# Optimization experiments

Hardware: AMD Instinct MI355X
Metric: run time of the kernel (lower is better)

## Reference

```python
import jax, jax.numpy as jnp
import numpy as np

T, B, D_IN, NHID = 4096, 8, 512, 512

def setup_inputs() -> dict:
    key = jax.random.key(0)
    k1, k2, k3 = jax.random.split(key, 3)
    scale_i = 1.0 / np.sqrt(D_IN)
    scale_h = 1.0 / np.sqrt(NHID)
    x = jax.random.normal(k1, (T, B, D_IN), dtype=jnp.float32)
    hidden0 = jnp.zeros((2, B, NHID), dtype=jnp.float32)  # [h; cell]
    Wi = jax.random.normal(k2, (D_IN, 4 * NHID), dtype=jnp.float32) * scale_i
    bi = jnp.zeros((4 * NHID,), dtype=jnp.float32)
    Wh = jax.random.normal(k3, (NHID, 4 * NHID), dtype=jnp.float32) * scale_h
    bh = jnp.zeros((4 * NHID,), dtype=jnp.float32)
    return {"x": x, "hidden0": hidden0, "Wi": Wi, "bi": bi, "Wh": Wh, "bh": bh}

def reference(x, hidden0, Wi, bi, Wh, bh):
    n = Wh.shape[0]

    def update(state, xt):
        h, cell = state[0], state[1]               # [B, n] each
        pre = xt @ Wi + bi + h @ Wh + bh           # [B, 4n]
        gates = jax.nn.sigmoid(pre[:, : 3 * n])
        forget_gate = gates[:, :n]
        input_gate = gates[:, n : 2 * n]
        output_gate = gates[:, 2 * n : 3 * n]
        new_cell = jnp.tanh(pre[:, 3 * n :])
        cell = forget_gate * cell + input_gate * new_cell
        h = output_gate * jnp.tanh(cell)
        return jnp.stack([h, cell]), h

    new_state, hidden_stacked = jax.lax.scan(update, hidden0, x)
    return hidden_stacked, new_state
```

## Files before the change

kernel.cpp:

```cpp
#include <hip/hip_runtime.h>
#include <hip/hip_bf16.h>

#define T_STEPS 4096
#define BATCH 8
#define DIN 512
#define NH 512
#define G4 2048
#define NWV 32
#define JPW 16

typedef __attribute__((ext_vector_type(8))) short bf16x8;
typedef __attribute__((ext_vector_type(4))) float f32x4;
typedef __attribute__((ext_vector_type(4))) int i32x4;

__device__ __forceinline__ unsigned short f2b(float f) {
  __hip_bfloat16 h = __float2bfloat16(f);
  return __builtin_bit_cast(unsigned short, h);
}
__device__ __forceinline__ float b2f(unsigned short u) {
  unsigned int x = ((unsigned int)u) << 16;
  return __builtin_bit_cast(float, x);
}
__device__ __forceinline__ float sigf(float x) { return 1.f / (1.f + __expf(-x)); }
__device__ __forceinline__ float tanh_fast(float x) { return 1.f - 2.f / (1.f + __expf(2.f * x)); }

__global__ __launch_bounds__(512) void init_ws(const float* __restrict__ h0,
                                               unsigned int* __restrict__ tags,
                                               unsigned short* __restrict__ hbuf) {
  int tid = threadIdx.x;
  if (tid < NWV) tags[tid] = 0u;
  for (int i = tid; i < 4096; i += 512) {
    int b = i >> 9, j = i & 511;
    hbuf[i] = f2b(h0[b * NH + j]);
    hbuf[4096 + i] = 0;
  }
}

#define BM 64
#define BN 64
#define BK 16
__global__ __launch_bounds__(256) void xi_gemm(const float* __restrict__ x,
                                               const float* __restrict__ Wi,
                                               const float* __restrict__ bi,
                                               const float* __restrict__ bh,
                                               unsigned short* __restrict__ xi) {
  __shared__ float As[BK][BM + 4];
  __shared__ float Bs[BK][BN + 4];
  const int tid = threadIdx.x;
  const int m0 = blockIdx.x * BM;
  const int n0 = blockIdx.y * BN;
  const int tx = tid & 15, ty = tid >> 4;
  const int arow = tid & 63, ak = (tid >> 6) << 2;
  const int bk = tid >> 4, bn = (tid & 15) << 2;
  float acc[4][4] = {};
  for (int k0 = 0; k0 < DIN; k0 += BK) {
    float4 av = *(const float4*)(x + (size_t)(m0 + arow) * DIN + k0 + ak);
    float4 bv = *(const float4*)(Wi + (size_t)(k0 + bk) * G4 + n0 + bn);
    __syncthreads();
    As[ak + 0][arow] = av.x;
    As[ak + 1][arow] = av.y;
    As[ak + 2][arow] = av.z;
    As[ak + 3][arow] = av.w;
    *(float4*)&Bs[bk][bn] = bv;
    __syncthreads();
#pragma unroll
    for (int kk = 0; kk < BK; ++kk) {
      float am[4], bw[4];
      *(float4*)am = *(const float4*)&As[kk][ty << 2];
      *(float4*)bw = *(const float4*)&Bs[kk][tx << 2];
#pragma unroll
      for (int i = 0; i < 4; ++i)
#pragma unroll
        for (int j = 0; j < 4; ++j) acc[i][j] = fmaf(am[i], bw[j], acc[i][j]);
    }
  }
  const int m_base = m0 + (ty << 2);
  const int n_base = n0 + (tx << 2);
  const int tt = m_base >> 3;
  const int rg = (m_base & 7) >> 2;
  const int gate = n_base >> 9;
  const int wv = (n_base & 511) >> 4;
  const int col0 = n_base & 15;
#pragma unroll
  for (int j = 0; j < 4; ++j) {
    int n = n_base + j;
    float bs = bi[n] + bh[n];
    unsigned long long pk = 0;
#pragma unroll
    for (int i = 0; i < 4; ++i)
      pk |= (unsigned long long)f2b(acc[i][j] + bs) << (16 * i);
    int lane = rg * 16 + col0 + j;
    size_t u16idx = (((size_t)tt * NWV + wv) * 32 + lane) * 16 + gate * 4;
    *(unsigned long long*)(xi + u16idx) = pk;
  }
}

__global__ __launch_bounds__(64, 1) void lstm_rec(const float* __restrict__ Wh,
                                                  const float* __restrict__ h0c0,
                                                  const unsigned short* __restrict__ xi,
                                                  float* __restrict__ out,
                                                  unsigned int* tags,
                                                  unsigned short* hbuf) {
  const int wv = blockIdx.x;
  const int j0 = wv * JPW;
  const int lane = threadIdx.x;
  const int col = lane & 15;
  const int rg = lane >> 4;

  __shared__ bf16x8 bwS[4][16][64];

  {
    const int gp = lane >> 4, cp = lane & 15;
    const float* wsrc = Wh + (size_t)gp * NH + j0 + cp;
#pragma unroll 4
    for (int k = 0; k < 512; ++k) {
      float wval = wsrc[(size_t)k * G4];
      const int ks = k >> 5, kq = (k >> 3) & 3, e = k & 7;
      ((unsigned short*)&bwS[gp][ks][kq * 16 + cp])[e] = f2b(wval);
    }
  }
  __syncthreads();

  bf16x8 bwR0[16], bwR1[16];
#pragma unroll
  for (int ks = 0; ks < 16; ++ks) {
    bwR0[ks] = bwS[0][ks][lane];
    bwR1[ks] = bwS[1][ks][lane];
  }

  f32x4 cell = {0.f, 0.f, 0.f, 0.f};
  if (lane < 32) {
#pragma unroll
    for (int q = 0; q < 4; ++q)
      cell[q] = h0c0[(size_t)(BATCH + rg * 4 + q) * NH + j0 + col];
  }

  i32x4 xiC0, xiC1, xiN0, xiN1;
  {
    const unsigned short* xp = xi + ((size_t)wv * 32 + (lane & 31)) * 16;
    asm volatile("global_load_dwordx4 %0, %1, off" : "=&v"(xiC0) : "v"(xp));
    asm volatile("global_load_dwordx4 %0, %1, off offset:16" : "=&v"(xiC1) : "v"(xp));
  }
  f32x4 hq = {0.f, 0.f, 0.f, 0.f};

  const unsigned int* tp = tags + (lane & 31);
  unsigned int* myTag = tags + wv;

  for (int t = 0; t < T_STEPS; ++t) {
    {
      unsigned int tv;
      do {
        asm volatile("global_load_dword %0, %1, off sc0 sc1\n\ts_waitcnt vmcnt(0)"
                     : "=v"(tv) : "v"(tp) : "memory");
      } while (__any((int)tv < t));
    }

    const unsigned short* mb = hbuf + ((t & 1) << 12);
    const unsigned short* ap = mb + (col & 7) * 512 + (rg << 3);
    i32x4 afr[16];
    asm volatile("global_load_dwordx4 %0, %1, off sc0 sc1" : "=v"(afr[0]) : "v"(ap));
    asm volatile("global_load_dwordx4 %0, %1, off offset:64 sc0 sc1" : "=v"(afr[1]) : "v"(ap));
    asm volatile("global_load_dwordx4 %0, %1, off offset:128 sc0 sc1" : "=v"(afr[2]) : "v"(ap));
    asm volatile("global_load_dwordx4 %0, %1, off offset:192 sc0 sc1" : "=v"(afr[3]) : "v"(ap));
    asm volatile("global_load_dwordx4 %0, %1, off offset:256 sc0 sc1" : "=v"(afr[4]) : "v"(ap));
    asm volatile("global_load_dwordx4 %0, %1, off offset:320 sc0 sc1" : "=v"(afr[5]) : "v"(ap));
    asm volatile("global_load_dwordx4 %0, %1, off offset:384 sc0 sc1" : "=v"(afr[6]) : "v"(ap));
    asm volatile("global_load_dwordx4 %0, %1, off offset:448 sc0 sc1" : "=v"(afr[7]) : "v"(ap));
    asm volatile("global_load_dwordx4 %0, %1, off offset:512 sc0 sc1" : "=v"(afr[8]) : "v"(ap));
    asm volatile("global_load_dwordx4 %0, %1, off offset:576 sc0 sc1" : "=v"(afr[9]) : "v"(ap));
    asm volatile("global_load_dwordx4 %0, %1, off offset:640 sc0 sc1" : "=v"(afr[10]) : "v"(ap));
    asm volatile("global_load_dwordx4 %0, %1, off offset:704 sc0 sc1" : "=v"(afr[11]) : "v"(ap));
    asm volatile("global_load_dwordx4 %0, %1, off offset:768 sc0 sc1" : "=v"(afr[12]) : "v"(ap));
    asm volatile("global_load_dwordx4 %0, %1, off offset:832 sc0 sc1" : "=v"(afr[13]) : "v"(ap));
    asm volatile("global_load_dwordx4 %0, %1, off offset:896 sc0 sc1" : "=v"(afr[14]) : "v"(ap));
    asm volatile("global_load_dwordx4 %0, %1, off offset:960 sc0 sc1" : "=v"(afr[15]) : "v"(ap));
    asm volatile("s_waitcnt vmcnt(0)" ::: "memory");
    __builtin_amdgcn_sched_barrier(0);

    f32x4 acc[4][2];
    {
      unsigned int wrd[8] = {(unsigned int)xiC0[0], (unsigned int)xiC0[1],
                             (unsigned int)xiC0[2], (unsigned int)xiC0[3],
                             (unsigned int)xiC1[0], (unsigned int)xiC1[1],
                             (unsigned int)xiC1[2], (unsigned int)xiC1[3]};
      f32x4 z = {0.f, 0.f, 0.f, 0.f};
#pragma unroll
      for (int g = 0; g < 4; ++g) {
#pragma unroll
        for (int q = 0; q < 4; ++q) {
          const int idx = g * 4 + q;
          acc[g][0][q] = b2f((unsigned short)(wrd[idx >> 1] >> ((idx & 1) * 16)));
        }
        acc[g][1] = z;
      }
    }
#pragma unroll
    for (int ks = 0; ks < 16; ++ks) {
      bf16x8 a = __builtin_bit_cast(bf16x8, afr[ks]);
      acc[0][ks & 1] = __builtin_amdgcn_mfma_f32_16x16x32_bf16(a, bwR0[ks], acc[0][ks & 1], 0, 0, 0);
      acc[1][ks & 1] = __builtin_amdgcn_mfma_f32_16x16x32_bf16(a, bwR1[ks], acc[1][ks & 1], 0, 0, 0);
      acc[2][ks & 1] = __builtin_amdgcn_mfma_f32_16x16x32_bf16(a, bwS[2][ks][lane], acc[2][ks & 1], 0, 0, 0);
      acc[3][ks & 1] = __builtin_amdgcn_mfma_f32_16x16x32_bf16(a, bwS[3][ks][lane], acc[3][ks & 1], 0, 0, 0);
    }

#pragma unroll
    for (int q = 0; q < 4; ++q) {
      float pf = acc[0][0][q] + acc[0][1][q];
      float pi = acc[1][0][q] + acc[1][1][q];
      float po = acc[2][0][q] + acc[2][1][q];
      float pg = acc[3][0][q] + acc[3][1][q];
      float fg = sigf(pf), ig = sigf(pi), og = sigf(po), gg = tanh_fast(pg);
      float cn = fg * cell[q] + ig * gg;
      cell[q] = cn;
      hq[q] = og * tanh_fast(cn);
    }

    if (lane < 32) {
      unsigned short* pp = hbuf + (((t + 1) & 1) << 12) + (rg * 4) * 512 + j0 + col;
      unsigned int h0u = f2b(hq[0]), h1u = f2b(hq[1]), h2u = f2b(hq[2]), h3u = f2b(hq[3]);
      asm volatile("global_store_short %0, %1, off sc0 sc1" :: "v"(pp), "v"(h0u) : "memory");
      asm volatile("global_store_short %0, %1, off offset:1024 sc0 sc1" :: "v"(pp), "v"(h1u) : "memory");
      asm volatile("global_store_short %0, %1, off offset:2048 sc0 sc1" :: "v"(pp), "v"(h2u) : "memory");
      asm volatile("global_store_short %0, %1, off offset:3072 sc0 sc1" :: "v"(pp), "v"(h3u) : "memory");
    }
    asm volatile("s_waitcnt vmcnt(0)" ::: "memory");
    if (lane == 0) {
      unsigned int tn1 = (unsigned int)(t + 1);
      asm volatile("global_store_dword %0, %1, off sc0 sc1" :: "v"(myTag), "v"(tn1) : "memory");
    }

    if (lane < 32) {
#pragma unroll
      for (int q = 0; q < 4; ++q)
        out[((size_t)t * BATCH + (rg * 4 + q)) * NH + j0 + col] = hq[q];
    }
    {
      const int tn = (t + 1 < T_STEPS) ? (t + 1) : t;
      const unsigned short* xp = xi + (((size_t)tn * NWV + wv) * 32 + (lane & 31)) * 16;
      asm volatile("global_load_dwordx4 %0, %1, off" : "=&v"(xiN0) : "v"(xp));
      asm volatile("global_load_dwordx4 %0, %1, off offset:16" : "=&v"(xiN1) : "v"(xp));
    }
    xiC0 = xiN0;
    xiC1 = xiN1;
  }

  if (lane < 32) {
    const size_t tail = (size_t)T_STEPS * BATCH * NH;
#pragma unroll
    for (int q = 0; q < 4; ++q) {
      out[tail + (size_t)(rg * 4 + q) * NH + j0 + col] = hq[q];
      out[tail + (size_t)BATCH * NH + (size_t)(rg * 4 + q) * NH + j0 + col] = cell[q];
    }
  }
}

extern "C" void kernel_launch(void* const* d_in, const int* in_sizes, int n_in,
                              void* d_out, int out_size, void* d_ws, size_t ws_size,
                              hipStream_t stream) {
  const float* x  = (const float*)d_in[0];
  const float* h0 = (const float*)d_in[1];
  const float* Wi = (const float*)d_in[2];
  const float* bi = (const float*)d_in[3];
  const float* Wh = (const float*)d_in[4];
  const float* bh = (const float*)d_in[5];
  float* out = (float*)d_out;

  unsigned int* tags = (unsigned int*)d_ws;
  unsigned short* hbuf = (unsigned short*)((char*)d_ws + 256);
  unsigned short* xi = (unsigned short*)((char*)d_ws + 65536);

  init_ws<<<1, 512, 0, stream>>>(h0, tags, hbuf);
  dim3 g1((T_STEPS * BATCH) / BM, G4 / BN);
  xi_gemm<<<g1, 256, 0, stream>>>(x, Wi, bi, bh, xi);
  lstm_rec<<<NWV, 64, 0, stream>>>(Wh, h0, xi, out, tags, hbuf);
}
```

Measured before the change: 15.11 ms.

## Replace flag polling with tagged mailbox carrying hidden state and step tag

Removes the separate per-workgroup tag array. Each published bf16 hidden pair is now stored next to its timestep tag in an 8-byte mailbox word, so consumers poll the data loads themselves and retry until every tag matches. This drops one round-trip (flag poll, then data load) per recurrent step. It also batches the output writes through shared memory, flushing 16 timesteps with float4 stores, and issues the next xi prefetch earlier. The costs are double the data loaded per poll and a bounded retry loop that gives up silently after 4096 rounds.

```diff
diff --git a/kernel.cpp b/kernel.cpp
--- a/kernel.cpp
+++ b/kernel.cpp
@@ -25,14 +25,14 @@
 __device__ __forceinline__ float tanh_fast(float x) { return 1.f - 2.f / (1.f + __expf(2.f * x)); }
 
 __global__ __launch_bounds__(512) void init_ws(const float* __restrict__ h0,
-                                               unsigned int* __restrict__ tags,
-                                               unsigned short* __restrict__ hbuf) {
+                                               unsigned long long* __restrict__ mbox) {
   int tid = threadIdx.x;
-  if (tid < NWV) tags[tid] = 0u;
-  for (int i = tid; i < 4096; i += 512) {
-    int b = i >> 9, j = i & 511;
-    hbuf[i] = f2b(h0[b * NH + j]);
-    hbuf[4096 + i] = 0;
+  for (int i = tid; i < 2048; i += 512) {
+    int b = i >> 8, m = i & 255;
+    unsigned int pk = ((unsigned int)f2b(h0[b * NH + 2 * m + 1]) << 16) |
+                      f2b(h0[b * NH + 2 * m]);
+    mbox[i] = (unsigned long long)pk;
+    mbox[2048 + i] = 0xFFFFFFFFull << 32;
   }
 }
 
@@ -99,8 +99,7 @@
                                                   const float* __restrict__ h0c0,
                                                   const unsigned short* __restrict__ xi,
                                                   float* __restrict__ out,
-                                                  unsigned int* tags,
-                                                  unsigned short* hbuf) {
+                                                  unsigned long long* mbox) {
   const int wv = blockIdx.x;
   const int j0 = wv * JPW;
   const int lane = threadIdx.x;
@@ -108,6 +107,7 @@
   const int rg = lane >> 4;
 
   __shared__ bf16x8 bwS[4][16][64];
+  __shared__ float obuf[16][8][16];
 
   {
     const int gp = lane >> 4, cp = lane & 15;
@@ -143,39 +143,55 @@
   }
   f32x4 hq = {0.f, 0.f, 0.f, 0.f};
 
-  const unsigned int* tp = tags + (lane & 31);
-  unsigned int* myTag = tags + wv;
+  const char* mbase = (const char*)mbox + (size_t)(col & 7) * 2048 + (size_t)rg * 32;
+  const int pb = lane >> 2, pu = lane & 3;
+  const int srcbase = ((pb >> 2) << 4) + (pu << 2);
+  const int qs = pb & 3;
+  char* pbase = (char*)mbox + (size_t)pb * 2048 + (size_t)j0 * 4 + (size_t)pu * 16;
+
+  i32x4 aL[16], aH[16];
 
   for (int t = 0; t < T_STEPS; ++t) {
+    const unsigned int tgt = (unsigned int)t;
+    const char* mb = mbase + ((t & 1) << 14);
+
+#define PL(i, o0, o1)                                                              \
+    asm volatile("global_load_dwordx4 %0, %1, off offset:" #o0 " sc0 sc1"          \
+                 : "=&v"(aL[i]) : "v"(mb));                                        \
+    asm volatile("global_load_dwordx4 %0, %1, off offset:" #o1 " sc0 sc1"          \
+                 : "=&v"(aH[i]) : "v"(mb));
+#define ISSUE_ALL                                                                  \
+    PL(0, 0, 16)       PL(1, 128, 144)    PL(2, 256, 272)    PL(3, 384, 400)       \
+    PL(4, 512, 528)    PL(5, 640, 656)    PL(6, 768, 784)    PL(7, 896, 912)       \
+    PL(8, 1024, 1040)  PL(9, 1152, 1168)  PL(10, 1280, 1296) PL(11, 1408, 1424)    \
+    PL(12, 1536, 1552) PL(13, 1664, 1680) PL(14, 1792, 1808) PL(15, 1920, 1936)
     {
-      unsigned int tv;
-      do {
-        asm volatile("global_load_dword %0, %1, off sc0 sc1\n\ts_waitcnt vmcnt(0)"
-                     : "=v"(tv) : "v"(tp) : "memory");
-      } while (__any((int)tv < t));
-    }
-
-    const unsigned short* mb = hbuf + ((t & 1) << 12);
-    const unsigned short* ap = mb + (col & 7) * 512 + (rg << 3);
-    i32x4 afr[16];
-    asm volatile("global_load_dwordx4 %0, %1, off sc0 sc1" : "=v"(afr[0]) : "v"(ap));
-    asm volatile("global_load_dwordx4 %0, %1, off offset:64 sc0 sc1" : "=v"(afr[1]) : "v"(ap));
-    asm volatile("global_load_dwordx4 %0, %1, off offset:128 sc0 sc1" : "=v"(afr[2]) : "v"(ap));
-    asm volatile("global_load_dwordx4 %0, %1, off offset:192 sc0 sc1" : "=v"(afr[3]) : "v"(ap));
-    asm volatile("global_load_dwordx4 %0, %1, off offset:256 sc0 sc1" : "=v"(afr[4]) : "v"(ap));
-    asm volatile("global_load_dwordx4 %0, %1, off offset:320 sc0 sc1" : "=v"(afr[5]) : "v"(ap));
-    asm volatile("global_load_dwordx4 %0, %1, off offset:384 sc0 sc1" : "=v"(afr[6]) : "v"(ap));
-    asm volatile("global_load_dwordx4 %0, %1, off offset:448 sc0 sc1" : "=v"(afr[7]) : "v"(ap));
-    asm volatile("global_load_dwordx4 %0, %1, off offset:512 sc0 sc1" : "=v"(afr[8]) : "v"(ap));
-    asm volatile("global_load_dwordx4 %0, %1, off offset:576 sc0 sc1" : "=v"(afr[9]) : "v"(ap));
-    asm volatile("global_load_dwordx4 %0, %1, off offset:640 sc0 sc1" : "=v"(afr[10]) : "v"(ap));
-    asm volatile("global_load_dwordx4 %0, %1, off offset:704 sc0 sc1" : "=v"(afr[11]) : "v"(ap));
-    asm volatile("global_load_dwordx4 %0, %1, off offset:768 sc0 sc1" : "=v"(afr[12]) : "v"(ap));
-    asm volatile("global_load_dwordx4 %0, %1, off offset:832 sc0 sc1" : "=v"(afr[13]) : "v"(ap));
-    asm volatile("global_load_dwordx4 %0, %1, off offset:896 sc0 sc1" : "=v"(afr[14]) : "v"(ap));
-    asm volatile("global_load_dwordx4 %0, %1, off offset:960 sc0 sc1" : "=v"(afr[15]) : "v"(ap));
-    asm volatile("s_waitcnt vmcnt(0)" ::: "memory");
-    __builtin_amdgcn_sched_barrier(0);
+      unsigned int bad;
+      int rounds = 0;
+      for (;;) {
+        ISSUE_ALL
+        asm volatile("s_waitcnt vmcnt(0)" ::: "memory");
+        __builtin_amdgcn_sched_barrier(0);
+        bad = 0u;
+#pragma unroll
+        for (int ks = 0; ks < 16; ++ks) {
+          bad |= ((unsigned int)aL[ks][1] ^ tgt) | ((unsigned int)aL[ks][3] ^ tgt) |
+                 ((unsigned int)aH[ks][1] ^ tgt) | ((unsigned int)aH[ks][3] ^ tgt);
+        }
+        if (__all(bad == 0u)) break;
+        if (++rounds > 4096) break;
+        if (rounds > 8) asm volatile("s_sleep 1");
+      }
+    }
+#undef PL
+#undef ISSUE_ALL
+
+    {
+      const int tn = (t + 1 < T_STEPS) ? (t + 1) : t;
+      const unsigned short* xp = xi + (((size_t)tn * NWV + wv) * 32 + (lane & 31)) * 16;
+      asm volatile("global_load_dwordx4 %0, %1, off" : "=&v"(xiN0) : "v"(xp));
+      asm volatile("global_load_dwordx4 %0, %1, off offset:16" : "=&v"(xiN1) : "v"(xp));
+    }
 
     f32x4 acc[4][2];
     {
@@ -196,7 +212,8 @@
     }
 #pragma unroll
     for (int ks = 0; ks < 16; ++ks) {
-      bf16x8 a = __builtin_bit_cast(bf16x8, afr[ks]);
+      i32x4 fr = {aL[ks][0], aL[ks][2], aH[ks][0], aH[ks][2]};
+      bf16x8 a = __builtin_bit_cast(bf16x8, fr);
       acc[0][ks & 1] = __builtin_amdgcn_mfma_f32_16x16x32_bf16(a, bwR0[ks], acc[0][ks & 1], 0, 0, 0);
       acc[1][ks & 1] = __builtin_amdgcn_mfma_f32_16x16x32_bf16(a, bwR1[ks], acc[1][ks & 1], 0, 0, 0);
       acc[2][ks & 1] = __builtin_amdgcn_mfma_f32_16x16x32_bf16(a, bwS[2][ks][lane], acc[2][ks & 1], 0, 0, 0);
@@ -215,30 +232,43 @@
       hq[q] = og * tanh_fast(cn);
     }
 
+    {
+      float v0 = 0.f, v1 = 0.f, v2 = 0.f, v3 = 0.f;
+#pragma unroll
+      for (int qq = 0; qq < 4; ++qq) {
+        float s0 = __shfl(hq[qq], srcbase + 0);
+        float s1 = __shfl(hq[qq], srcbase + 1);
+        float s2 = __shfl(hq[qq], srcbase + 2);
+        float s3 = __shfl(hq[qq], srcbase + 3);
+        if (qq == qs) { v0 = s0; v1 = s1; v2 = s2; v3 = s3; }
+      }
+      if (lane < 32) {
+        unsigned int tag1 = (unsigned int)(t + 1);
+        i32x4 pub;
+        pub[0] = (int)(((unsigned int)f2b(v1) << 16) | f2b(v0));
+        pub[1] = (int)tag1;
+        pub[2] = (int)(((unsigned int)f2b(v3) << 16) | f2b(v2));
+        pub[3] = (int)tag1;
+        char* pp = pbase + (((t + 1) & 1) << 14);
+        asm volatile("global_store_dwordx4 %0, %1, off sc0 sc1" :: "v"(pp), "v"(pub) : "memory");
+      }
+    }
+    asm volatile("s_waitcnt vmcnt(0)" ::: "memory");
+
     if (lane < 32) {
-      unsigned short* pp = hbuf + (((t + 1) & 1) << 12) + (rg * 4) * 512 + j0 + col;
-      unsigned int h0u = f2b(hq[0]), h1u = f2b(hq[1]), h2u = f2b(hq[2]), h3u = f2b(hq[3]);
-      asm volatile("global_store_short %0, %1, off sc0 sc1" :: "v"(pp), "v"(h0u) : "memory");
-      asm volatile("global_store_short %0, %1, off offset:1024 sc0 sc1" :: "v"(pp), "v"(h1u) : "memory");
-      asm volatile("global_store_short %0, %1, off offset:2048 sc0 sc1" :: "v"(pp), "v"(h2u) : "memory");
-      asm volatile("global_store_short %0, %1, off offset:3072 sc0 sc1" :: "v"(pp), "v"(h3u) : "memory");
-    }
-    asm volatile("s_waitcnt vmcnt(0)" ::: "memory");
-    if (lane == 0) {
-      unsigned int tn1 = (unsigned int)(t + 1);
-      asm volatile("global_store_dword %0, %1, off sc0 sc1" :: "v"(myTag), "v"(tn1) : "memory");
-    }
-
-    if (lane < 32) {
-#pragma unroll
-      for (int q = 0; q < 4; ++q)
-        out[((size_t)t * BATCH + (rg * 4 + q)) * NH + j0 + col] = hq[q];
-    }
-    {
-      const int tn = (t + 1 < T_STEPS) ? (t + 1) : t;
-      const unsigned short* xp = xi + (((size_t)tn * NWV + wv) * 32 + (lane & 31)) * 16;
-      asm volatile("global_load_dwordx4 %0, %1, off" : "=&v"(xiN0) : "v"(xp));
-      asm volatile("global_load_dwordx4 %0, %1, off offset:16" : "=&v"(xiN1) : "v"(xp));
+      const int st = t & 15;
+#pragma unroll
+      for (int q = 0; q < 4; ++q) obuf[st][rg * 4 + q][col] = hq[q];
+    }
+    if ((t & 15) == 15) {
+      const int t0 = t - 15;
+#pragma unroll
+      for (int it = 0; it < 8; ++it) {
+        const int run = (lane >> 2) + it * 16;
+        const int st = run >> 3, b = run & 7, jj = (lane & 3) << 2;
+        float4 v = *(const float4*)&obuf[st][b][jj];
+        *(float4*)(out + ((size_t)(t0 + st) * BATCH + b) * NH + j0 + jj) = v;
+      }
     }
     xiC0 = xiN0;
     xiC1 = xiN1;
@@ -265,12 +295,11 @@
   const float* bh = (const float*)d_in[5];
   float* out = (float*)d_out;
 
-  unsigned int* tags = (unsigned int*)d_ws;
-  unsigned short* hbuf = (unsigned short*)((char*)d_ws + 256);
+  unsigned long long* mbox = (unsigned long long*)d_ws;
   unsigned short* xi = (unsigned short*)((char*)d_ws + 65536);
 
-  init_ws<<<1, 512, 0, stream>>>(h0, tags, hbuf);
+  init_ws<<<1, 512, 0, stream>>>(h0, mbox);
   dim3 g1((T_STEPS * BATCH) / BM, G4 / BN);
   xi_gemm<<<g1, 256, 0, stream>>>(x, Wi, bi, bh, xi);
-  lstm_rec<<<NWV, 64, 0, stream>>>(Wh, h0, xi, out, tags, hbuf);
-}
+  lstm_rec<<<NWV, 64, 0, stream>>>(Wh, h0, xi, out, mbox);
+}
```

Measured after the change: 21.47 ms. +42.1%, slower.
